# Kernel optimization log

Hardware: AMD Instinct MI355X
Metric: run time of the kernel (lower is better)

## Reference

```python
import jax, jax.numpy as jnp
import numpy as np
import math

B, N, D = 4, 16384, 256
M, H = 64, 8
HD = D // H

def setup_inputs() -> dict:
    key = jax.random.key(0)
    ks = jax.random.split(key, 5)
    s = 1.0 / math.sqrt(D)
    return {
        "x": jax.random.normal(ks[0], (B, N, D), dtype=jnp.float32),
        "Ws": jax.random.normal(ks[1], (M, D), dtype=jnp.float32) * s,
        "bs": jnp.zeros((M,), dtype=jnp.float32),
        "Wqkv": jax.random.normal(ks[2], (3 * D, D), dtype=jnp.float32) * s,
        "Wo": jax.random.normal(ks[3], (D, D), dtype=jnp.float32) * s,
        "bo": jnp.zeros((D,), dtype=jnp.float32),
    }

def reference(x, Ws, bs, Wqkv, Wo, bo):
    # slice weights: softmax over N (dim=1), matching the torch code exactly
    logits = jnp.einsum('bnd,md->bnm', x, Ws) + bs          # [B,N,M]
    weights = jax.nn.softmax(logits, axis=1)                # softmax over N
    # pooling: tokens[b,m,d] = sum_n w[b,n,m] * x[b,n,d]
    tokens = jnp.einsum('bnm,bnd->bmd', weights, x)         # [B,M,D]
    # qkv projection (no bias)
    qkv = jnp.einsum('bmd,ed->bme', tokens, Wqkv)           # [B,M,3D]
    qkv = qkv.reshape(B, M, 3, H, HD)
    q = qkv[:, :, 0].transpose(0, 2, 1, 3)                  # [B,H,M,HD]
    k = qkv[:, :, 1].transpose(0, 2, 1, 3)
    v = qkv[:, :, 2].transpose(0, 2, 1, 3)
    scale = 1.0 / math.sqrt(HD)
    attn = jax.nn.softmax(jnp.einsum('bhmd,bhkd->bhmk', q, k) * scale, axis=-1)
    token_out = jnp.einsum('bhmk,bhkd->bhmd', attn, v)      # [B,H,M,HD]
    token_out = token_out.transpose(0, 2, 1, 3).reshape(B, M, D)
    token_out = jnp.einsum('bmd,ed->bme', token_out, Wo) + bo
    # unpooling: out[b,n,d] = sum_m w[b,n,m] * token_out[b,m,d]
    out = jnp.einsum('bnm,bmd->bnd', weights, token_out)    # [B,N,D]
    return out
```

## Files before the change

kernel.cpp:

```cpp
#include <hip/hip_runtime.h>
#include <math.h>

constexpr int B = 4;
constexpr int N = 16384;
constexpr int D = 256;
constexpr int M = 64;
constexpr int H = 8;

typedef __attribute__((ext_vector_type(8))) short short8;
typedef __attribute__((ext_vector_type(4))) float floatx4;

__device__ __forceinline__ float4 ld4(const float* p) {
  return *reinterpret_cast<const float4*>(p);
}
__device__ __forceinline__ unsigned short f2bf(float f) {
  unsigned u = __float_as_uint(f);
  unsigned r = (u + 0x7fffu + ((u >> 16) & 1u)) >> 16;
  return (unsigned short)r;
}

__global__ __launch_bounds__(256) void k0_prep(
    const float* __restrict__ Ws, const float* __restrict__ Wqkv,
    const float* __restrict__ Wo, unsigned short* __restrict__ WsB,
    unsigned short* __restrict__ WqkvB, unsigned short* __restrict__ WoB,
    float* __restrict__ denom, float* __restrict__ tokens,
    float* __restrict__ tokO) {
  const int g = blockIdx.x * 256 + threadIdx.x;
  if (g < 32768) {
    *reinterpret_cast<float2*>(&tokens[g * 2]) = make_float2(0.f, 0.f);
    *reinterpret_cast<float2*>(&tokO[g * 2]) = make_float2(0.f, 0.f);
  }
  if (g < 128)
    *reinterpret_cast<float2*>(&denom[g * 2]) = make_float2(0.f, 0.f);
  const float* src;
  unsigned short* dst;
  int off;
  if (g < 2048) {
    src = Ws; dst = WsB; off = g;
  } else if (g < 26624) {
    src = Wqkv; dst = WqkvB; off = g - 2048;
  } else {
    src = Wo; dst = WoB; off = g - 26624;
  }
  const float4 a = ld4(&src[(size_t)off * 8]);
  const float4 c = ld4(&src[(size_t)off * 8 + 4]);
  unsigned d0 = (unsigned)f2bf(a.x) | ((unsigned)f2bf(a.y) << 16);
  unsigned d1 = (unsigned)f2bf(a.z) | ((unsigned)f2bf(a.w) << 16);
  unsigned d2 = (unsigned)f2bf(c.x) | ((unsigned)f2bf(c.y) << 16);
  unsigned d3 = (unsigned)f2bf(c.z) | ((unsigned)f2bf(c.w) << 16);
  *reinterpret_cast<uint4*>(&dst[(size_t)off * 8]) = make_uint4(d0, d1, d2, d3);
}

__global__ __launch_bounds__(256, 2) void k12_fused(
    const float* __restrict__ x, const unsigned short* __restrict__ WsB,
    const float* __restrict__ bs, unsigned short* __restrict__ En,
    float* __restrict__ denom, float* __restrict__ tokens) {
  __shared__ unsigned short Wt[64][264];
  __shared__ unsigned short EsT[64][70];
  __shared__ unsigned short XsT[256][70];
  __shared__ float red[64];
  const int b = blockIdx.y;
  const int nb0 = blockIdx.x * 128;
  const int tid = threadIdx.x;
  const int w = tid >> 6, l = tid & 63;
  const int l15 = l & 15;
  const int q8 = (l >> 4) * 8;
  const int r4 = (l >> 4) * 4;
  const int ar = w * 16 + l15;

  float4 fx0[16];
  {
    const float* xr = &x[((size_t)(b * N + nb0 + ar)) * D];
#pragma unroll
    for (int ks = 0; ks < 8; ++ks) {
      fx0[2 * ks] = ld4(&xr[ks * 32 + q8]);
      fx0[2 * ks + 1] = ld4(&xr[ks * 32 + q8 + 4]);
    }
  }
#pragma unroll
  for (int p = 0; p < 8; ++p) {
    const int u = p * 256 + tid;
    const int row = u >> 5;
    const int c = (u & 31) * 8;
    *reinterpret_cast<short8*>(&Wt[row][c]) =
        *reinterpret_cast<const short8*>(&WsB[(size_t)row * 256 + c]);
  }
  if (tid < 64) red[tid] = 0.0f;
  __syncthreads();

  floatx4 acc2[16];
#pragma unroll
  for (int i = 0; i < 16; ++i) acc2[i] = {0.f, 0.f, 0.f, 0.f};

  float4 fx1[16];
  short8 afr[8];
  floatx4 acc[4];

#define K12_CVT(FX)                                                    \
  do {                                                                 \
    _Pragma("unroll") for (int ks = 0; ks < 8; ++ks) {                 \
      const float4 a0 = FX[2 * ks], a1 = FX[2 * ks + 1];               \
      short8 tt;                                                       \
      tt[0] = (short)f2bf(a0.x); tt[1] = (short)f2bf(a0.y);            \
      tt[2] = (short)f2bf(a0.z); tt[3] = (short)f2bf(a0.w);            \
      tt[4] = (short)f2bf(a1.x); tt[5] = (short)f2bf(a1.y);            \
      tt[6] = (short)f2bf(a1.z); tt[7] = (short)f2bf(a1.w);            \
      afr[ks] = tt;                                                    \
    }                                                                  \
  } while (0)

#define K12_SCATTER()                                                  \
  do {                                                                 \
    _Pragma("unroll") for (int ks = 0; ks < 8; ++ks)                   \
        _Pragma("unroll") for (int j = 0; j < 8; ++j)                  \
            XsT[ks * 32 + q8 + j][ar] = (unsigned short)afr[ks][j];    \
  } while (0)

#define K12_LOGITS()                                                   \
  do {                                                                 \
    _Pragma("unroll") for (int i = 0; i < 4; ++i)                      \
        acc[i] = {0.f, 0.f, 0.f, 0.f};                                 \
    _Pragma("unroll") for (int ks = 0; ks < 8; ++ks) {                 \
      _Pragma("unroll") for (int mt = 0; mt < 4; ++mt) {               \
        short8 bf =                                                    \
            *reinterpret_cast<short8*>(&Wt[mt * 16 + l15][ks * 32 + q8]); \
        acc[mt] = __builtin_amdgcn_mfma_f32_16x16x32_bf16(afr[ks], bf, \
                                                          acc[mt], 0, 0, 0); \
      }                                                                \
    }                                                                  \
  } while (0)

#define K12_EPILOG(N0)                                                 \
  do {                                                                 \
    _Pragma("unroll") for (int mt = 0; mt < 4; ++mt) {                 \
      const int m = mt * 16 + l15;                                     \
      const float bsm = bs[m];                                         \
      float s = 0.0f;                                                  \
      _Pragma("unroll") for (int r = 0; r < 4; ++r) {                  \
        const int n = w * 16 + r4 + r;                                 \
        const float e = __expf(acc[mt][r] + bsm);                      \
        s += e;                                                        \
        const unsigned short eb = f2bf(e);                             \
        EsT[m][w * 16 + r4 + r] = eb;                                  \
        En[((size_t)(b * N + (N0) + n)) * M + m] = eb;                 \
      }                                                                \
      atomicAdd(&red[m], s);                                           \
    }                                                                  \
  } while (0)

#define K12_POOL()                                                     \
  do {                                                                 \
    _Pragma("unroll") for (int ks2 = 0; ks2 < 2; ++ks2) {              \
      const int nf = ks2 * 32 + q8;                                    \
      short8 a = *reinterpret_cast<short8*>(&EsT[w * 16 + l15][nf]);   \
      _Pragma("unroll") for (int dt4 = 0; dt4 < 16; ++dt4) {           \
        short8 bf = *reinterpret_cast<short8*>(&XsT[dt4 * 16 + l15][nf]); \
        acc2[dt4] = __builtin_amdgcn_mfma_f32_16x16x32_bf16(a, bf,     \
                                                            acc2[dt4], 0, 0, 0); \
      }                                                                \
    }                                                                  \
  } while (0)

  K12_CVT(fx0);
  {
    const float* xr = &x[((size_t)(b * N + nb0 + 64 + ar)) * D];
#pragma unroll
    for (int ks = 0; ks < 8; ++ks) {
      fx1[2 * ks] = ld4(&xr[ks * 32 + q8]);
      fx1[2 * ks + 1] = ld4(&xr[ks * 32 + q8 + 4]);
    }
  }
  K12_SCATTER();
  K12_LOGITS();
  K12_EPILOG(nb0);
  __syncthreads();
  K12_POOL();
  __syncthreads();

  K12_CVT(fx1);
  K12_SCATTER();
  K12_LOGITS();
  K12_EPILOG(nb0 + 64);
  __syncthreads();
  K12_POOL();

  if (tid < 64) atomicAdd(&denom[b * M + tid], red[tid]);
#pragma unroll
  for (int dt4 = 0; dt4 < 16; ++dt4)
#pragma unroll
    for (int r = 0; r < 4; ++r) {
      const int m = w * 16 + r4 + r;
      const int d = dt4 * 16 + l15;
      atomicAdd(&tokens[((size_t)(b * M + m)) * D + d], acc2[dt4][r]);
    }
#undef K12_CVT
#undef K12_SCATTER
#undef K12_LOGITS
#undef K12_EPILOG
#undef K12_POOL
}

__global__ __launch_bounds__(256) void k_fa(
    const float* __restrict__ tokens, const unsigned short* __restrict__ WqkvB,
    const unsigned short* __restrict__ WoB, const float* __restrict__ denom,
    float* __restrict__ tokO) {
  __shared__ __align__(16) char smem[84480];
  unsigned short* const At = reinterpret_cast<unsigned short*>(smem);
  unsigned short* const Wq = reinterpret_cast<unsigned short*>(smem + 33792);
  float* const qt = reinterpret_cast<float*>(smem);
  float* const kt = reinterpret_cast<float*>(smem + 8704);
  float* const vv = reinterpret_cast<float*>(smem + 17408);
  float* const P  = reinterpret_cast<float*>(smem + 26624);
  float* const ao = reinterpret_cast<float*>(smem + 44032);
  const int b = blockIdx.x >> 3;
  const int h = blockIdx.x & 7;
  const int tid = threadIdx.x;
  const int w = tid >> 6, l = tid & 63;
  const int l15 = l & 15;
  const int q8 = (l >> 4) * 8;
  const int r4 = (l >> 4) * 4;

#pragma unroll
  for (int p = 0; p < 16; ++p) {
    const int i = p * 256 + tid;
    const int row = i >> 6;
    const int c4 = (i & 63) * 4;
    float4 av = ld4(&tokens[((size_t)(b * M + row)) * D + c4]);
    unsigned a0 = (unsigned)f2bf(av.x) | ((unsigned)f2bf(av.y) << 16);
    unsigned a1 = (unsigned)f2bf(av.z) | ((unsigned)f2bf(av.w) << 16);
    *reinterpret_cast<uint2*>(&At[row * 264 + c4]) = make_uint2(a0, a1);
  }
#pragma unroll
  for (int p = 0; p < 12; ++p) {
    const int u = p * 256 + tid;
    const int row = u >> 5;
    const int c = (u & 31) * 8;
    const int eg = (row < 32) ? (h * 32 + row)
                 : (row < 64) ? (256 + h * 32 + row - 32)
                              : (512 + h * 32 + row - 64);
    *reinterpret_cast<short8*>(&Wq[row * 264 + c]) =
        *reinterpret_cast<const short8*>(&WqkvB[(size_t)eg * 256 + c]);
  }
  float rcp4[4];
#pragma unroll
  for (int r = 0; r < 4; ++r)
    rcp4[r] = 1.0f / denom[b * M + w * 16 + r4 + r];
  __syncthreads();

  floatx4 acc[6] = {{0.f, 0.f, 0.f, 0.f}, {0.f, 0.f, 0.f, 0.f},
                    {0.f, 0.f, 0.f, 0.f}, {0.f, 0.f, 0.f, 0.f},
                    {0.f, 0.f, 0.f, 0.f}, {0.f, 0.f, 0.f, 0.f}};
  const int arow = w * 16 + l15;
#pragma unroll
  for (int ks = 0; ks < 8; ++ks) {
    short8 a = *reinterpret_cast<short8*>(&At[arow * 264 + ks * 32 + q8]);
#pragma unroll
    for (int et = 0; et < 6; ++et) {
      short8 bf = *reinterpret_cast<short8*>(&Wq[(et * 16 + l15) * 264 + ks * 32 + q8]);
      acc[et] = __builtin_amdgcn_mfma_f32_16x16x32_bf16(a, bf, acc[et], 0, 0, 0);
    }
  }
  short8 wof[4];
#pragma unroll
  for (int dt4 = 0; dt4 < 4; ++dt4)
    wof[dt4] = *reinterpret_cast<const short8*>(
        &WoB[(size_t)(w * 64 + dt4 * 16 + l15) * 256 + h * 32 + q8]);
  __syncthreads();

#pragma unroll
  for (int r = 0; r < 4; ++r) {
    const int m = w * 16 + r4 + r;
    const float rc = rcp4[r];
#pragma unroll
    for (int et = 0; et < 6; ++et) {
      const float val = acc[et][r] * rc;
      const int c = (et & 1) * 16 + l15;
      if (et < 2) qt[c * 68 + m] = val;
      else if (et < 4) kt[c * 68 + m] = val;
      else vv[m * 36 + c] = val;
    }
  }
  __syncthreads();

  {
    const int tm4 = (tid & 15) * 4;
    const int tn4 = (tid >> 4) * 4;
    float sacc[4][4] = {};
    for (int k = 0; k < 32; ++k) {
      float4 a4 = ld4(&qt[k * 68 + tn4]);
      float4 b4 = ld4(&kt[k * 68 + tm4]);
#pragma unroll
      for (int i = 0; i < 4; ++i) {
        const float av = (i == 0) ? a4.x : (i == 1) ? a4.y : (i == 2) ? a4.z : a4.w;
        sacc[i][0] = fmaf(av, b4.x, sacc[i][0]);
        sacc[i][1] = fmaf(av, b4.y, sacc[i][1]);
        sacc[i][2] = fmaf(av, b4.z, sacc[i][2]);
        sacc[i][3] = fmaf(av, b4.w, sacc[i][3]);
      }
    }
    const float scale = 0.17677669529663687f;
#pragma unroll
    for (int i = 0; i < 4; ++i)
      *reinterpret_cast<float4*>(&P[(tn4 + i) * 68 + tm4]) =
          make_float4(sacc[i][0] * scale, sacc[i][1] * scale,
                      sacc[i][2] * scale, sacc[i][3] * scale);
  }
  __syncthreads();
  if (tid < 64) {
    float mx = -1e30f;
    for (int j = 0; j < 64; ++j) mx = fmaxf(mx, P[tid * 68 + j]);
    float s = 0.0f;
    for (int j = 0; j < 64; ++j) {
      const float e = expf(P[tid * 68 + j] - mx);
      P[tid * 68 + j] = e;
      s += e;
    }
    const float r = 1.0f / s;
    for (int j = 0; j < 64; ++j) P[tid * 68 + j] *= r;
  }
  __syncthreads();
  if (tid < 128) {
    const int i0 = (tid >> 3) * 4;
    const int c0 = (tid & 7) * 4;
    float o[4][4] = {};
    for (int j = 0; j < 64; ++j) {
      float4 v4 = ld4(&vv[j * 36 + c0]);
#pragma unroll
      for (int ii = 0; ii < 4; ++ii) {
        const float p = P[(i0 + ii) * 68 + j];
        o[ii][0] = fmaf(p, v4.x, o[ii][0]);
        o[ii][1] = fmaf(p, v4.y, o[ii][1]);
        o[ii][2] = fmaf(p, v4.z, o[ii][2]);
        o[ii][3] = fmaf(p, v4.w, o[ii][3]);
      }
    }
#pragma unroll
    for (int ii = 0; ii < 4; ++ii)
#pragma unroll
      for (int jj = 0; jj < 4; ++jj) ao[(i0 + ii) * 36 + c0 + jj] = o[ii][jj];
  }
  __syncthreads();

  floatx4 acc2[4][4] = {{{0.f, 0.f, 0.f, 0.f}, {0.f, 0.f, 0.f, 0.f},
                         {0.f, 0.f, 0.f, 0.f}, {0.f, 0.f, 0.f, 0.f}},
                        {{0.f, 0.f, 0.f, 0.f}, {0.f, 0.f, 0.f, 0.f},
                         {0.f, 0.f, 0.f, 0.f}, {0.f, 0.f, 0.f, 0.f}},
                        {{0.f, 0.f, 0.f, 0.f}, {0.f, 0.f, 0.f, 0.f},
                         {0.f, 0.f, 0.f, 0.f}, {0.f, 0.f, 0.f, 0.f}},
                        {{0.f, 0.f, 0.f, 0.f}, {0.f, 0.f, 0.f, 0.f},
                         {0.f, 0.f, 0.f, 0.f}, {0.f, 0.f, 0.f, 0.f}}};
#pragma unroll
  for (int mt = 0; mt < 4; ++mt) {
    short8 af;
#pragma unroll
    for (int j = 0; j < 8; ++j)
      af[j] = (short)f2bf(ao[(mt * 16 + l15) * 36 + q8 + j]);
#pragma unroll
    for (int dt4 = 0; dt4 < 4; ++dt4)
      acc2[mt][dt4] =
          __builtin_amdgcn_mfma_f32_16x16x32_bf16(af, wof[dt4], acc2[mt][dt4], 0, 0, 0);
  }
#pragma unroll
  for (int mt = 0; mt < 4; ++mt)
#pragma unroll
    for (int dt4 = 0; dt4 < 4; ++dt4)
#pragma unroll
      for (int r = 0; r < 4; ++r) {
        const int m = mt * 16 + r4 + r;
        const int d = w * 64 + dt4 * 16 + l15;
        atomicAdd(&tokO[((size_t)(b * M + m)) * D + d], acc2[mt][dt4][r]);
      }
}

__global__ __launch_bounds__(512, 4) void k6_unpool(
    const unsigned short* __restrict__ En, const float* __restrict__ tokO,
    const float* __restrict__ denom, const float* __restrict__ bo,
    float* __restrict__ out) {
  __shared__ unsigned short EnS[128][72];
  __shared__ unsigned short TpS[64][72];
  const int dt = blockIdx.x, nt = blockIdx.y, b = blockIdx.z;
  const int n0 = nt * 128, d0 = dt * 64;
  const int tid = threadIdx.x;
  const int w = tid >> 6, l = tid & 63;
  const int l15 = l & 15;
  const int q8 = (l >> 4) * 8;
#pragma unroll
  for (int p = 0; p < 2; ++p) {
    const int g = p * 512 + tid;
    const int row = g >> 3;
    const int c8 = (g & 7) * 8;
    *reinterpret_cast<short8*>(&EnS[row][c8]) =
        *reinterpret_cast<const short8*>(
            &En[((size_t)(b * N + n0 + row)) * M + c8]);
  }
  {
    const int m = tid >> 3;
    const int c8 = (tid & 7) * 8;
    const float rc = 1.0f / denom[b * M + m];
    const float* tp = &tokO[((size_t)(b * M + m)) * D + d0 + c8];
    float4 v0 = ld4(tp);
    float4 v1 = ld4(tp + 4);
    float4 bb0 = ld4(&bo[d0 + c8]);
    float4 bb1 = ld4(&bo[d0 + c8 + 4]);
    TpS[c8 + 0][m] = f2bf((v0.x + bb0.x) * rc);
    TpS[c8 + 1][m] = f2bf((v0.y + bb0.y) * rc);
    TpS[c8 + 2][m] = f2bf((v0.z + bb0.z) * rc);
    TpS[c8 + 3][m] = f2bf((v0.w + bb0.w) * rc);
    TpS[c8 + 4][m] = f2bf((v1.x + bb1.x) * rc);
    TpS[c8 + 5][m] = f2bf((v1.y + bb1.y) * rc);
    TpS[c8 + 6][m] = f2bf((v1.z + bb1.z) * rc);
    TpS[c8 + 7][m] = f2bf((v1.w + bb1.w) * rc);
  }
  __syncthreads();
  floatx4 acc[4] = {{0.f, 0.f, 0.f, 0.f},
                    {0.f, 0.f, 0.f, 0.f},
                    {0.f, 0.f, 0.f, 0.f},
                    {0.f, 0.f, 0.f, 0.f}};
  const int arow = w * 16 + l15;
#pragma unroll
  for (int ks = 0; ks < 2; ++ks) {
    short8 a = *reinterpret_cast<short8*>(&EnS[arow][ks * 32 + q8]);
#pragma unroll
    for (int dtile = 0; dtile < 4; ++dtile) {
      short8 bf = *reinterpret_cast<short8*>(
          &TpS[dtile * 16 + l15][ks * 32 + q8]);
      acc[dtile] =
          __builtin_amdgcn_mfma_f32_16x16x32_bf16(a, bf, acc[dtile], 0, 0, 0);
    }
  }
#pragma unroll
  for (int dtile = 0; dtile < 4; ++dtile)
#pragma unroll
    for (int r = 0; r < 4; ++r) {
      const int n = n0 + w * 16 + (l >> 4) * 4 + r;
      const int d = d0 + dtile * 16 + l15;
      out[((size_t)(b * N + n)) * D + d] = acc[dtile][r];
    }
}

extern "C" void kernel_launch(void* const* d_in, const int* in_sizes, int n_in,
                              void* d_out, int out_size, void* d_ws,
                              size_t ws_size, hipStream_t stream) {
  const float* x = (const float*)d_in[0];
  const float* Ws = (const float*)d_in[1];
  const float* bs = (const float*)d_in[2];
  const float* Wqkv = (const float*)d_in[3];
  const float* Wo = (const float*)d_in[4];
  const float* bo = (const float*)d_in[5];
  float* out = (float*)d_out;

  char* p = (char*)d_ws;
  unsigned short* En = (unsigned short*)p;    p += (size_t)B * N * M * 2;
  float* denom = (float*)p;                   p += (size_t)B * M * 4;
  float* tokens = (float*)p;                  p += (size_t)B * M * D * 4;
  float* tokO = (float*)p;                    p += (size_t)B * M * D * 4;
  unsigned short* WsB = (unsigned short*)p;   p += (size_t)M * D * 2;
  unsigned short* WqkvB = (unsigned short*)p; p += (size_t)3 * D * D * 2;
  unsigned short* WoB = (unsigned short*)p;   p += (size_t)D * D * 2;

  k0_prep<<<dim3(136), 256, 0, stream>>>(Ws, Wqkv, Wo, WsB, WqkvB, WoB,
                                         denom, tokens, tokO);
  k12_fused<<<dim3(N / 128, B), 256, 0, stream>>>(x, WsB, bs, En, denom,
                                                  tokens);
  k_fa<<<dim3(B * H), 256, 0, stream>>>(tokens, WqkvB, WoB, denom, tokO);
  k6_unpool<<<dim3(D / 64, N / 128, B), 512, 0, stream>>>(En, tokO, denom, bo,
                                                          out);
}
```

Baseline: 174.4 us.

## Replace pooled-token atomics with per-block partial slots and a separate reduce kernel

Each k12_fused block now writes its 64x256 pooled partial sums to a private slot, where before it issued global float atomicAdds into tokens. A new k2r_reduce kernel then sums the 128 slots per batch. The second tile's bf16 conversion also moves earlier, before the barrier, to overlap it with pooling, using a second fragment register array. The change removes heavy atomic contention at the cost of 32MB of extra partial-sum writes and reads, an extra kernel launch, and more register pressure.

```diff
diff --git a/kernel.cpp b/kernel.cpp
--- a/kernel.cpp
+++ b/kernel.cpp
@@ -6,6 +6,7 @@
 constexpr int D = 256;
 constexpr int M = 64;
 constexpr int H = 8;
+constexpr int NSLOT = 128;
 
 typedef __attribute__((ext_vector_type(8))) short short8;
 typedef __attribute__((ext_vector_type(4))) float floatx4;
@@ -23,13 +24,10 @@
     const float* __restrict__ Ws, const float* __restrict__ Wqkv,
     const float* __restrict__ Wo, unsigned short* __restrict__ WsB,
     unsigned short* __restrict__ WqkvB, unsigned short* __restrict__ WoB,
-    float* __restrict__ denom, float* __restrict__ tokens,
-    float* __restrict__ tokO) {
+    float* __restrict__ denom, float* __restrict__ tokO) {
   const int g = blockIdx.x * 256 + threadIdx.x;
-  if (g < 32768) {
-    *reinterpret_cast<float2*>(&tokens[g * 2]) = make_float2(0.f, 0.f);
+  if (g < 32768)
     *reinterpret_cast<float2*>(&tokO[g * 2]) = make_float2(0.f, 0.f);
-  }
   if (g < 128)
     *reinterpret_cast<float2*>(&denom[g * 2]) = make_float2(0.f, 0.f);
   const float* src;
@@ -54,7 +52,7 @@
 __global__ __launch_bounds__(256, 2) void k12_fused(
     const float* __restrict__ x, const unsigned short* __restrict__ WsB,
     const float* __restrict__ bs, unsigned short* __restrict__ En,
-    float* __restrict__ denom, float* __restrict__ tokens) {
+    float* __restrict__ denom, float* __restrict__ tokensP) {
   __shared__ unsigned short Wt[64][264];
   __shared__ unsigned short EsT[64][70];
   __shared__ unsigned short XsT[256][70];
@@ -93,10 +91,10 @@
   for (int i = 0; i < 16; ++i) acc2[i] = {0.f, 0.f, 0.f, 0.f};
 
   float4 fx1[16];
-  short8 afr[8];
+  short8 afr0[8], afr1[8];
   floatx4 acc[4];
 
-#define K12_CVT(FX)                                                    \
+#define K12_CVT(FX, AFR)                                               \
   do {                                                                 \
     _Pragma("unroll") for (int ks = 0; ks < 8; ++ks) {                 \
       const float4 a0 = FX[2 * ks], a1 = FX[2 * ks + 1];               \
@@ -105,18 +103,18 @@
       tt[2] = (short)f2bf(a0.z); tt[3] = (short)f2bf(a0.w);            \
       tt[4] = (short)f2bf(a1.x); tt[5] = (short)f2bf(a1.y);            \
       tt[6] = (short)f2bf(a1.z); tt[7] = (short)f2bf(a1.w);            \
-      afr[ks] = tt;                                                    \
+      AFR[ks] = tt;                                                    \
     }                                                                  \
   } while (0)
 
-#define K12_SCATTER()                                                  \
+#define K12_SCATTER(AFR)                                               \
   do {                                                                 \
     _Pragma("unroll") for (int ks = 0; ks < 8; ++ks)                   \
         _Pragma("unroll") for (int j = 0; j < 8; ++j)                  \
-            XsT[ks * 32 + q8 + j][ar] = (unsigned short)afr[ks][j];    \
+            XsT[ks * 32 + q8 + j][ar] = (unsigned short)AFR[ks][j];    \
   } while (0)
 
-#define K12_LOGITS()                                                   \
+#define K12_LOGITS(AFR)                                                \
   do {                                                                 \
     _Pragma("unroll") for (int i = 0; i < 4; ++i)                      \
         acc[i] = {0.f, 0.f, 0.f, 0.f};                                 \
@@ -124,7 +122,7 @@
       _Pragma("unroll") for (int mt = 0; mt < 4; ++mt) {               \
         short8 bf =                                                    \
             *reinterpret_cast<short8*>(&Wt[mt * 16 + l15][ks * 32 + q8]); \
-        acc[mt] = __builtin_amdgcn_mfma_f32_16x16x32_bf16(afr[ks], bf, \
+        acc[mt] = __builtin_amdgcn_mfma_f32_16x16x32_bf16(AFR[ks], bf, \
                                                           acc[mt], 0, 0, 0); \
       }                                                                \
     }                                                                  \
@@ -161,7 +159,7 @@
     }                                                                  \
   } while (0)
 
-  K12_CVT(fx0);
+  K12_CVT(fx0, afr0);
   {
     const float* xr = &x[((size_t)(b * N + nb0 + 64 + ar)) * D];
 #pragma unroll
@@ -170,34 +168,49 @@
       fx1[2 * ks + 1] = ld4(&xr[ks * 32 + q8 + 4]);
     }
   }
-  K12_SCATTER();
-  K12_LOGITS();
+  K12_SCATTER(afr0);
+  K12_LOGITS(afr0);
   K12_EPILOG(nb0);
+  K12_CVT(fx1, afr1);
   __syncthreads();
   K12_POOL();
   __syncthreads();
 
-  K12_CVT(fx1);
-  K12_SCATTER();
-  K12_LOGITS();
+  K12_SCATTER(afr1);
+  K12_LOGITS(afr1);
   K12_EPILOG(nb0 + 64);
   __syncthreads();
   K12_POOL();
 
   if (tid < 64) atomicAdd(&denom[b * M + tid], red[tid]);
+  float* op = tokensP + ((size_t)(b * NSLOT + blockIdx.x) * M) * D;
 #pragma unroll
   for (int dt4 = 0; dt4 < 16; ++dt4)
 #pragma unroll
-    for (int r = 0; r < 4; ++r) {
-      const int m = w * 16 + r4 + r;
-      const int d = dt4 * 16 + l15;
-      atomicAdd(&tokens[((size_t)(b * M + m)) * D + d], acc2[dt4][r]);
-    }
+    for (int r = 0; r < 4; ++r)
+      op[(w * 16 + r4 + r) * D + dt4 * 16 + l15] = acc2[dt4][r];
 #undef K12_CVT
 #undef K12_SCATTER
 #undef K12_LOGITS
 #undef K12_EPILOG
 #undef K12_POOL
+}
+
+__global__ __launch_bounds__(256) void k2r_reduce(
+    const float* __restrict__ tokensP, float* __restrict__ tokens) {
+  const int b = blockIdx.x >> 6;
+  const int m = blockIdx.x & 63;
+  const int d = threadIdx.x;
+  const float* base = tokensP + ((size_t)(b * NSLOT) * M + m) * D + d;
+  float s0 = 0.f, s1 = 0.f, s2 = 0.f, s3 = 0.f;
+#pragma unroll 4
+  for (int s = 0; s < NSLOT; s += 4) {
+    s0 += base[(size_t)(s + 0) * M * D];
+    s1 += base[(size_t)(s + 1) * M * D];
+    s2 += base[(size_t)(s + 2) * M * D];
+    s3 += base[(size_t)(s + 3) * M * D];
+  }
+  tokens[((size_t)(b * M) + m) * D + d] = (s0 + s1) + (s2 + s3);
 }
 
 __global__ __launch_bounds__(256) void k_fa(
@@ -454,14 +467,16 @@
   float* denom = (float*)p;                   p += (size_t)B * M * 4;
   float* tokens = (float*)p;                  p += (size_t)B * M * D * 4;
   float* tokO = (float*)p;                    p += (size_t)B * M * D * 4;
+  float* tokensP = (float*)p;                 p += (size_t)B * NSLOT * M * D * 4;
   unsigned short* WsB = (unsigned short*)p;   p += (size_t)M * D * 2;
   unsigned short* WqkvB = (unsigned short*)p; p += (size_t)3 * D * D * 2;
   unsigned short* WoB = (unsigned short*)p;   p += (size_t)D * D * 2;
 
   k0_prep<<<dim3(136), 256, 0, stream>>>(Ws, Wqkv, Wo, WsB, WqkvB, WoB,
-                                         denom, tokens, tokO);
+                                         denom, tokO);
   k12_fused<<<dim3(N / 128, B), 256, 0, stream>>>(x, WsB, bs, En, denom,
-                                                  tokens);
+                                                  tokensP);
+  k2r_reduce<<<dim3(B * M), 256, 0, stream>>>(tokensP, tokens);
   k_fa<<<dim3(B * H), 256, 0, stream>>>(tokens, WqkvB, WoB, denom, tokO);
   k6_unpool<<<dim3(D / 64, N / 128, B), 512, 0, stream>>>(En, tokO, denom, bo,
                                                           out);
```

Measured after the change: 168.6 us. -3.3%, faster.
